# Optimization experiments

Measured on AMD Instinct MI355X. Metric: run time of the kernel, lower is better.

Reference implementation:

```python
import jax, jax.numpy as jnp
import numpy as np

N = 100000   # nodes (src == dst count)
E = 800000   # edges
D = 64       # hidden_dim == out_channels per head
H = 4        # heads
ED = 2       # edge_dim
NEG_SLOPE = 0.2
EPS = 1e-16


def setup_inputs() -> dict:
    key = jax.random.key(0)
    ks = jax.random.split(key, 12)
    s = 1.0 / np.sqrt(D)
    return {
        "x_src": jax.random.normal(ks[0], (N, D), jnp.float32),
        "x_dst": jax.random.normal(ks[1], (N, D), jnp.float32),
        "edge_index": jax.random.randint(ks[2], (2, E), 0, N),
        "edge_attr": jax.random.normal(ks[3], (E, ED), jnp.float32),
        "gamma": jnp.ones((D,), jnp.float32),
        "beta": jnp.zeros((D,), jnp.float32),
        "W_l": jax.random.normal(ks[4], (D, H * D), jnp.float32) * s,
        "b_l": jnp.zeros((H * D,), jnp.float32),
        "W_r": jax.random.normal(ks[5], (D, H * D), jnp.float32) * s,
        "b_r": jnp.zeros((H * D,), jnp.float32),
        "W_e": jax.random.normal(ks[6], (ED, H * D), jnp.float32) * s,
        "att": jax.random.normal(ks[7], (H, D), jnp.float32) * s,
        "bias": jnp.zeros((D,), jnp.float32),
    }


def _layernorm(x, gamma, beta):
    mu = jnp.mean(x, axis=-1, keepdims=True)
    var = jnp.var(x, axis=-1, keepdims=True)
    return (x - mu) * jax.lax.rsqrt(var + 1e-5) * gamma + beta


def reference(x_src, x_dst, edge_index, edge_attr, gamma, beta,
              W_l, b_l, W_r, b_r, W_e, att, bias):
    # shared LayerNorm on both bipartite node sets
    xs = _layernorm(x_src, gamma, beta)
    xd = _layernorm(x_dst, gamma, beta)
    # per-node linear transforms -> [N, H, D]
    hl = (xs @ W_l + b_l).reshape(N, H, D)   # source transform
    hr = (xd @ W_r + b_r).reshape(N, H, D)   # destination transform
    he = (edge_attr @ W_e).reshape(E, H, D)  # edge transform (no bias)
    src, dst = edge_index[0], edge_index[1]
    # GATv2 score: LeakyReLU(x_j + x_i + e) . att
    m = jax.nn.leaky_relu(hl[src] + hr[dst] + he, NEG_SLOPE)  # [E, H, D]
    alpha = jnp.einsum('ehd,hd->eh', m, att)                  # [E, H]
    # segment softmax over edges sharing a destination
    amax = jax.ops.segment_max(alpha, dst, num_segments=N)    # [N, H]
    ex = jnp.exp(alpha - amax[dst])
    denom = jax.ops.segment_sum(ex, dst, num_segments=N)      # [N, H]
    alpha = ex / (denom[dst] + EPS)
    # scatter-aggregate messages x_j * alpha
    out = jax.ops.segment_sum(hl[src] * alpha[..., None], dst, num_segments=N)  # [N, H, D]
    # concat=False -> mean over heads, then bias
    return out.mean(axis=1) + bias
```

## Files before the change

kernel.cpp:

```cpp
#include <hip/hip_runtime.h>
#include <hip/hip_bf16.h>
#include <cstdint>

#define NN 100000
#define EE 800000
#define DD 64
#define HH 4
#define HDIM 256
#define NEG 0.2f
#define L2E 1.4426950408889634f
#define CAP 44
#define HLMASK 0x03FFFFF8

#define NGB ((NN + 63) / 64)
#define GEMM_BLOCKS (NGB * 2)
#define SCAT_BLOCKS ((EE + 255) / 256)
#define SCAT4_BLOCKS ((EE + 1023) / 1024)
#define TOTAL_BLOCKS (SCAT4_BLOCKS * 5)

typedef __attribute__((ext_vector_type(8))) short bf16x8;
typedef __attribute__((ext_vector_type(4))) float f32x4;
typedef __attribute__((ext_vector_type(2))) float f32x2;

__device__ __forceinline__ float bf2f(unsigned short u) {
  union { unsigned int i; float f; } c; c.i = ((unsigned int)u) << 16; return c.f;
}
__device__ __forceinline__ unsigned short f2bf(float f) {
  union { float f; unsigned int i; } c; c.f = f;
  unsigned int r = c.i + 0x7FFF + ((c.i >> 16) & 1);
  return (unsigned short)(r >> 16);
}
__device__ __forceinline__ unsigned int pack2(unsigned short a, unsigned short b) {
  return (unsigned int)a | ((unsigned int)b << 16);
}
__device__ __forceinline__ f32x2 unpk(unsigned int u) {
  union { unsigned int i; float f; } lo, hi;
  lo.i = u << 16; hi.i = u & 0xffff0000u;
  f32x2 r; r.x = lo.f; r.y = hi.f; return r;
}
__device__ __forceinline__ f32x2 abs2(f32x2 a) {
  f32x2 r; r.x = fmaxf(a.x, -a.x); r.y = fmaxf(a.y, -a.y); return r;
}

#if __has_builtin(__builtin_amdgcn_exp2f)
#define EXP2F(x) __builtin_amdgcn_exp2f(x)
#else
#define EXP2F(x) exp2f(x)
#endif

#define ROWSUM16(p) do {                                                         \
  p += __int_as_float(__builtin_amdgcn_update_dpp(0, __float_as_int(p), 0x121, 0xF, 0xF, false)); \
  p += __int_as_float(__builtin_amdgcn_update_dpp(0, __float_as_int(p), 0x122, 0xF, 0xF, false)); \
  p += __int_as_float(__builtin_amdgcn_update_dpp(0, __float_as_int(p), 0x124, 0xF, 0xF, false)); \
  p += __int_as_float(__builtin_amdgcn_update_dpp(0, __float_as_int(p), 0x128, 0xF, 0xF, false)); \
} while (0)

#define CIDX(l) ((((l) >> 4) << 6) + (((l) & 3) << 4) + ((((l) >> 2) & 3) << 2))

__device__ __forceinline__ void prep_body(
    int mat,
    const float* __restrict__ W_l, const float* __restrict__ b_l,
    const float* __restrict__ W_r, const float* __restrict__ b_r,
    const float* __restrict__ gamma, const float* __restrict__ beta,
    unsigned short* __restrict__ Wgt, float* __restrict__ cw,
    float* __restrict__ cb)
{
  const int c = threadIdx.x;
  const float* W = mat ? W_r : W_l;
  const float* bb = mat ? b_r : b_l;
  unsigned short* wout = Wgt + (size_t)mat * HDIM * DD + (size_t)c * DD;
  float s_cw = 0.f, s_cb = 0.f;
#pragma unroll 8
  for (int k = 0; k < DD; ++k) {
    float wv = W[k * HDIM + c];
    unsigned short u = f2bf(gamma[k] * wv);
    wout[k] = u;
    s_cw += bf2f(u);
    s_cb += beta[k] * wv;
  }
  cw[mat * HDIM + c] = s_cw;
  cb[mat * HDIM + c] = s_cb + bb[c];
}

__global__ __launch_bounds__(256) void k_prep(
    const float* __restrict__ W_l, const float* __restrict__ b_l,
    const float* __restrict__ W_r, const float* __restrict__ b_r,
    const float* __restrict__ gamma, const float* __restrict__ beta,
    unsigned short* __restrict__ Wgt, float* __restrict__ cw,
    float* __restrict__ cb, int* __restrict__ deg)
{
  if (blockIdx.x < 2) {
    prep_body(blockIdx.x, W_l, b_l, W_r, b_r, gamma, beta, Wgt, cw, cb);
    return;
  }
  int i = (blockIdx.x - 2) * 256 + threadIdx.x;
  if (i < NN) deg[i] = 0;
}

__device__ __forceinline__ void gemm_body(
    int gx,
    const float* __restrict__ x_src, const float* __restrict__ x_dst,
    const unsigned short* __restrict__ Wgt, const float* __restrict__ cw,
    const float* __restrict__ cb,
    unsigned short* __restrict__ hl, unsigned short* __restrict__ hr)
{
  const int mat = gx & 1;
  const int tile = gx >> 1;
  const int t = threadIdx.x;
  const float* __restrict__ xp = mat ? x_dst : x_src;
  unsigned short* __restrict__ HM = mat ? hr : hl;

  __shared__ __align__(16) unsigned short sh[2][64 * 72];
  __shared__ float smu[64], sinv[64];

  const int l = t & 63, w = t >> 6;
  const int row16 = l & 15, hq = l >> 4;
  const int c0 = w * 64;

  const int sr = t >> 2, sq = t & 3;
  float v[16];
  {
    const int n = tile * 64 + sr;
    if (n < NN) {
      const f32x4* xr = (const f32x4*)(xp + (size_t)n * DD + sq * 16);
#pragma unroll
      for (int j = 0; j < 4; ++j) {
        f32x4 f = __builtin_nontemporal_load(xr + j);
        v[4 * j + 0] = f.x; v[4 * j + 1] = f.y;
        v[4 * j + 2] = f.z; v[4 * j + 3] = f.w;
      }
    } else {
#pragma unroll
      for (int j = 0; j < 16; ++j) v[j] = 0.f;
    }
  }

  const unsigned short* WgtM = Wgt + (size_t)mat * HDIM * DD;
  bf16x8 bfr[4][2];
#pragma unroll
  for (int cbk = 0; cbk < 4; ++cbk)
#pragma unroll
    for (int kb = 0; kb < 2; ++kb)
      bfr[cbk][kb] = *(const bf16x8*)(WgtM + (size_t)(c0 + cbk * 16 + row16) * DD
                                      + kb * 32 + hq * 8);
  float4 cw4[4], cb4[4];
#pragma unroll
  for (int cbk = 0; cbk < 4; ++cbk) {
    cw4[cbk] = *(const float4*)(cw + mat * HDIM + c0 + cbk * 16 + hq * 4);
    cb4[cbk] = *(const float4*)(cb + mat * HDIM + c0 + cbk * 16 + hq * 4);
  }

  {
    float s = 0.f, s2 = 0.f;
#pragma unroll
    for (int j = 0; j < 16; ++j) { s += v[j]; s2 += v[j] * v[j]; }
    s  += __shfl_xor(s, 1, 64);  s  += __shfl_xor(s, 2, 64);
    s2 += __shfl_xor(s2, 1, 64); s2 += __shfl_xor(s2, 2, 64);
    const float mu = s * (1.0f / DD);
    const float var = s2 * (1.0f / DD) - mu * mu;
    const float inv = rsqrtf(var + 1e-5f);
    if (sq == 0) { smu[sr] = mu; sinv[sr] = inv; }
    unsigned short hi[16], lo[16];
#pragma unroll
    for (int j = 0; j < 16; ++j) {
      unsigned short h = f2bf(v[j]);
      hi[j] = h;
      lo[j] = f2bf(v[j] - bf2f(h));
    }
    const int base = sr * 72 + sq * 16;
    uint4 w0, w1;
    w0.x = pack2(hi[0], hi[1]);  w0.y = pack2(hi[2], hi[3]);
    w0.z = pack2(hi[4], hi[5]);  w0.w = pack2(hi[6], hi[7]);
    w1.x = pack2(hi[8], hi[9]);  w1.y = pack2(hi[10], hi[11]);
    w1.z = pack2(hi[12], hi[13]); w1.w = pack2(hi[14], hi[15]);
    *(uint4*)(&sh[0][base]) = w0;
    *(uint4*)(&sh[0][base + 8]) = w1;
    w0.x = pack2(lo[0], lo[1]);  w0.y = pack2(lo[2], lo[3]);
    w0.z = pack2(lo[4], lo[5]);  w0.w = pack2(lo[6], lo[7]);
    w1.x = pack2(lo[8], lo[9]);  w1.y = pack2(lo[10], lo[11]);
    w1.z = pack2(lo[12], lo[13]); w1.w = pack2(lo[14], lo[15]);
    *(uint4*)(&sh[1][base]) = w0;
    *(uint4*)(&sh[1][base + 8]) = w1;
  }
  __syncthreads();

#pragma unroll
  for (int rb = 0; rb < 4; ++rb) {
    const int abase = (rb * 16 + row16) * 72 + hq * 8;
    bf16x8 xh0 = *(const bf16x8*)(&sh[0][abase]);
    bf16x8 xh1 = *(const bf16x8*)(&sh[0][abase + 32]);
    bf16x8 xl0 = *(const bf16x8*)(&sh[1][abase]);
    bf16x8 xl1 = *(const bf16x8*)(&sh[1][abase + 32]);
    f32x4 acc[4];
#pragma unroll
    for (int cbk = 0; cbk < 4; ++cbk) {
      acc[cbk] = (f32x4){0.f, 0.f, 0.f, 0.f};
      acc[cbk] = __builtin_amdgcn_mfma_f32_16x16x32_bf16(bfr[cbk][0], xh0, acc[cbk], 0, 0, 0);
      acc[cbk] = __builtin_amdgcn_mfma_f32_16x16x32_bf16(bfr[cbk][1], xh1, acc[cbk], 0, 0, 0);
      acc[cbk] = __builtin_amdgcn_mfma_f32_16x16x32_bf16(bfr[cbk][0], xl0, acc[cbk], 0, 0, 0);
      acc[cbk] = __builtin_amdgcn_mfma_f32_16x16x32_bf16(bfr[cbk][1], xl1, acc[cbk], 0, 0, 0);
    }
    const int nloc = rb * 16 + row16;
    const int node = tile * 64 + nloc;
    const float mu = smu[nloc], inv = sinv[nloc];
    if (node < NN) {
      float hh[4][4];
#pragma unroll
      for (int cbk = 0; cbk < 4; ++cbk) {
        hh[cbk][0] = fmaf(-mu, cw4[cbk].x, acc[cbk][0]) * inv + cb4[cbk].x;
        hh[cbk][1] = fmaf(-mu, cw4[cbk].y, acc[cbk][1]) * inv + cb4[cbk].y;
        hh[cbk][2] = fmaf(-mu, cw4[cbk].z, acc[cbk][2]) * inv + cb4[cbk].z;
        hh[cbk][3] = fmaf(-mu, cw4[cbk].w, acc[cbk][3]) * inv + cb4[cbk].w;
      }
      unsigned short* rp = HM + (size_t)node * HDIM + c0 + hq * 16;
      uint4 s0, s1;
      s0.x = pack2(f2bf(hh[0][0]), f2bf(hh[0][1]));
      s0.y = pack2(f2bf(hh[0][2]), f2bf(hh[0][3]));
      s0.z = pack2(f2bf(hh[1][0]), f2bf(hh[1][1]));
      s0.w = pack2(f2bf(hh[1][2]), f2bf(hh[1][3]));
      s1.x = pack2(f2bf(hh[2][0]), f2bf(hh[2][1]));
      s1.y = pack2(f2bf(hh[2][2]), f2bf(hh[2][3]));
      s1.z = pack2(f2bf(hh[3][0]), f2bf(hh[3][1]));
      s1.w = pack2(f2bf(hh[3][2]), f2bf(hh[3][3]));
      *(uint4*)rp = s0;
      *(uint4*)(rp + 8) = s1;
    }
  }
}

__device__ __forceinline__ void scatter_body4(
    int bx, const int* __restrict__ ei, const float* __restrict__ eattr,
    int* __restrict__ deg, int2* __restrict__ epack)
{
  const int e0 = bx * 1024 + threadIdx.x;
  int src[4], dst[4];
  unsigned long long ea[4];
  bool ok[4];
#pragma unroll
  for (int k = 0; k < 4; ++k) {
    const int e = e0 + k * 256;
    ok[k] = (e < EE);
    const int es = ok[k] ? e : 0;
    src[k] = __builtin_nontemporal_load(ei + es);
    dst[k] = __builtin_nontemporal_load(ei + EE + es);
    ea[k]  = __builtin_nontemporal_load((const unsigned long long*)(eattr + 2 * es));
  }
  int slot[4];
#pragma unroll
  for (int k = 0; k < 4; ++k) {
    if (ok[k]) slot[k] = atomicAdd(&deg[dst[k]], 1);
    else slot[k] = CAP;
  }
#pragma unroll
  for (int k = 0; k < 4; ++k) {
    if (slot[k] < CAP) {
      const float eax = __uint_as_float((unsigned int)ea[k]);
      const float eay = __uint_as_float((unsigned int)(ea[k] >> 32));
      unsigned long long rec =
          (unsigned long long)(unsigned int)(src[k] << 9)
          | ((unsigned long long)pack2(f2bf(eax), f2bf(eay)) << 32);
      __builtin_nontemporal_store(
          rec, (unsigned long long*)(epack + (size_t)dst[k] * CAP + slot[k]));
    }
  }
}

__global__ __launch_bounds__(256) void k_gemm_scatter(
    const float* __restrict__ x_src, const float* __restrict__ x_dst,
    const unsigned short* __restrict__ Wgt, const float* __restrict__ cw,
    const float* __restrict__ cb,
    unsigned short* __restrict__ hl, unsigned short* __restrict__ hr,
    const int* __restrict__ ei, const float* __restrict__ eattr,
    int* __restrict__ deg, int2* __restrict__ epack)
{
  const int bx = blockIdx.x;
  const int q = bx / 5, r = bx - q * 5;
  if (r == 4) {
    scatter_body4(q, ei, eattr, deg, epack);
  } else {
    const int g = q * 4 + r;
    if (g < GEMM_BLOCKS)
      gemm_body(g, x_src, x_dst, Wgt, cw, cb, hl, hr);
  }
}

__global__ __launch_bounds__(256, 8) void k_agg(
    const int* __restrict__ deg,
    const unsigned short* __restrict__ hl, const unsigned short* __restrict__ hr,
    const float* __restrict__ W_e, const float* __restrict__ att,
    const float* __restrict__ bias, const int2* __restrict__ epack,
    float* __restrict__ out)
{
  const int t = threadIdx.x;
  const int l = t & 63;
  const int loff = l * 8;
  const int cidx = CIDX(l);
  const char* hlb = (const char*)hl;

  const float4 at4 = *(const float4*)(att + cidx);
  const float4 w0  = *(const float4*)(W_e + cidx);
  const float4 w1  = *(const float4*)(W_e + HDIM + cidx);
  f32x2 atA01, atA23, atB01, atB23, w001, w023, w101, w123;
  atA01.x = at4.x * (0.6f * L2E); atA01.y = at4.y * (0.6f * L2E);
  atA23.x = at4.z * (0.6f * L2E); atA23.y = at4.w * (0.6f * L2E);
  atB01.x = at4.x * (0.4f * L2E); atB01.y = at4.y * (0.4f * L2E);
  atB23.x = at4.z * (0.4f * L2E); atB23.y = at4.w * (0.4f * L2E);
  w001.x = w0.x; w001.y = w0.y; w023.x = w0.z; w023.y = w0.w;
  w101.x = w1.x; w101.y = w1.y; w123.x = w1.z; w123.y = w1.w;

  const int nwaves = gridDim.x * (blockDim.x >> 6);
  const int wid0 = blockIdx.x * (blockDim.x >> 6) + (t >> 6);
  for (int n = wid0; n < NN; n += nwaves) {
    const int nu = __builtin_amdgcn_readfirstlane(n);
    int cnt = __builtin_amdgcn_readfirstlane(deg[nu]);
    cnt = min(cnt, CAP);
    const uint2 hv = *(const uint2*)(hr + (size_t)nu * HDIM + l * 4);
    const f32x2 r01 = unpk(hv.x), r23 = unpk(hv.y);
    f32x2 acc01 = {0.f, 0.f}, acc23 = {0.f, 0.f};
    float den = 0.f;

    auto EDGE = [&](int ey, uint2 av) {
      const f32x2 eav = unpk((unsigned int)ey);
      const f32x2 a01 = unpk(av.x), a23 = unpk(av.y);
      f32x2 s01 = a01 + r01 + w001 * eav.x + w101 * eav.y;
      f32x2 s23 = a23 + r23 + w023 * eav.x + w123 * eav.y;
      f32x2 q = s01 * atA01 + abs2(s01) * atB01;
      q = q + s23 * atA23 + abs2(s23) * atB23;
      float p = q.x + q.y;
      ROWSUM16(p);
      const float ex = EXP2F(p);
      acc01 += a01 * ex;
      acc23 += a23 * ex;
      den += ex;
    };

    if (cnt > 0) {
      const int2* eptr = epack + (size_t)nu * CAP;
      int2 e0 = eptr[0], e1 = eptr[1], e2 = eptr[2], e3 = eptr[3],
           e4 = eptr[4], e5 = eptr[5], e6 = eptr[6], e7 = eptr[7];
      uint2 a0 = *(const uint2*)(hlb + (e0.x & HLMASK) + loff);
      uint2 a1 = *(const uint2*)(hlb + (e1.x & HLMASK) + loff);
      uint2 a2 = *(const uint2*)(hlb + (e2.x & HLMASK) + loff);
      uint2 a3 = *(const uint2*)(hlb + (e3.x & HLMASK) + loff);
      int i = 0;
      for (; i + 4 <= cnt; i += 4) {
        uint2 b4 = *(const uint2*)(hlb + (e4.x & HLMASK) + loff);
        uint2 b5 = *(const uint2*)(hlb + (e5.x & HLMASK) + loff);
        uint2 b6 = *(const uint2*)(hlb + (e6.x & HLMASK) + loff);
        uint2 b7 = *(const uint2*)(hlb + (e7.x & HLMASK) + loff);
        int2 t0 = eptr[i + 8], t1 = eptr[i + 9],
             t2 = eptr[i + 10], t3 = eptr[i + 11];
        EDGE(e0.y, a0);
        EDGE(e1.y, a1);
        EDGE(e2.y, a2);
        EDGE(e3.y, a3);
        e0 = e4; e1 = e5; e2 = e6; e3 = e7;
        e4 = t0; e5 = t1; e6 = t2; e7 = t3;
        a0 = b4; a1 = b5; a2 = b6; a3 = b7;
      }
      const int rem = cnt - i;
      if (rem > 0) EDGE(e0.y, a0);
      if (rem > 1) EDGE(e1.y, a1);
      if (rem > 2) EDGE(e2.y, a2);
    }

    const float inv = 1.0f / (den + 1e-16f);
    float v0 = acc01.x * inv, v1 = acc01.y * inv;
    float v2 = acc23.x * inv, v3 = acc23.y * inv;
    v0 += __shfl_xor(v0, 16, 64); v0 += __shfl_xor(v0, 32, 64);
    v1 += __shfl_xor(v1, 16, 64); v1 += __shfl_xor(v1, 32, 64);
    v2 += __shfl_xor(v2, 16, 64); v2 += __shfl_xor(v2, 32, 64);
    v3 += __shfl_xor(v3, 16, 64); v3 += __shfl_xor(v3, 32, 64);
    if (l < 16) {
      const float4 bias4 = *(const float4*)(bias + cidx);
      float4 o;
      o.x = 0.25f * v0 + bias4.x;
      o.y = 0.25f * v1 + bias4.y;
      o.z = 0.25f * v2 + bias4.z;
      o.w = 0.25f * v3 + bias4.w;
      *(float4*)(out + (size_t)nu * DD + cidx) = o;
    }
  }
}

__global__ __launch_bounds__(256) void k_prep_count(
    const float* __restrict__ W_l, const float* __restrict__ b_l,
    const float* __restrict__ W_r, const float* __restrict__ b_r,
    const float* __restrict__ gamma, const float* __restrict__ beta,
    unsigned short* __restrict__ Wgt, float* __restrict__ cw,
    float* __restrict__ cb,
    const int* __restrict__ ei, int* __restrict__ counts)
{
  if (blockIdx.x < 2) {
    prep_body(blockIdx.x, W_l, b_l, W_r, b_r, gamma, beta, Wgt, cw, cb);
  } else {
    int e = (blockIdx.x - 2) * 256 + threadIdx.x;
    if (e < EE) atomicAdd(&counts[ei[EE + e]], 1);
  }
}

__global__ __launch_bounds__(256) void k_base(const int* __restrict__ counts,
                                              int* __restrict__ cursor,
                                              int* __restrict__ rowstart,
                                              int* __restrict__ cur) {
  const int lane = threadIdx.x & 63;
  const int wid = (blockIdx.x * blockDim.x + threadIdx.x) >> 6;
  const int n = wid * 64 + lane;
  int val = (n < NN) ? counts[n] : 0;
  int s = val;
#pragma unroll
  for (int off = 1; off < 64; off <<= 1) {
    int tsh = __shfl_up(s, off, 64);
    if (lane >= off) s += tsh;
  }
  int total = __shfl(s, 63, 64);
  int base = 0;
  if (lane == 0) base = atomicAdd(cursor, total);
  base = __shfl(base, 0, 64);
  if (n < NN) {
    int rs = base + s - val;
    rowstart[n] = rs;
    cur[n] = rs;
  }
}

__global__ __launch_bounds__(256) void k_scatter_csr(const int* __restrict__ ei,
                                                     const float* __restrict__ eattr,
                                                     int* __restrict__ cur,
                                                     int2* __restrict__ epack) {
  int e = blockIdx.x * blockDim.x + threadIdx.x;
  if (e >= EE) return;
  if (e < 64) epack[EE + e] = make_int2(0, 0);
  int src = ei[e];
  int dst = ei[EE + e];
  float2 ea = *(const float2*)(eattr + 2 * e);
  int pos = atomicAdd(&cur[dst], 1);
  epack[pos] = make_int2(src << 9, (int)pack2(f2bf(ea.x), f2bf(ea.y)));
}

__global__ __launch_bounds__(256, 8) void k_agg_csr(
    const int* __restrict__ rowstart, const int* __restrict__ counts,
    const unsigned short* __restrict__ hl, const unsigned short* __restrict__ hr,
    const float* __restrict__ W_e, const float* __restrict__ att,
    const float* __restrict__ bias, const int2* __restrict__ epack,
    float* __restrict__ out)
{
  const int t = threadIdx.x;
  const int l = t & 63;
  const int loff = l * 8;
  const int cidx = CIDX(l);
  const char* hlb = (const char*)hl;
  const float4 at4 = *(const float4*)(att + cidx);
  const float4 w0  = *(const float4*)(W_e + cidx);
  const float4 w1  = *(const float4*)(W_e + HDIM + cidx);
  f32x2 atA01, atA23, atB01, atB23, w001, w023, w101, w123;
  atA01.x = at4.x * (0.6f * L2E); atA01.y = at4.y * (0.6f * L2E);
  atA23.x = at4.z * (0.6f * L2E); atA23.y = at4.w * (0.6f * L2E);
  atB01.x = at4.x * (0.4f * L2E); atB01.y = at4.y * (0.4f * L2E);
  atB23.x = at4.z * (0.4f * L2E); atB23.y = at4.w * (0.4f * L2E);
  w001.x = w0.x; w001.y = w0.y; w023.x = w0.z; w023.y = w0.w;
  w101.x = w1.x; w101.y = w1.y; w123.x = w1.z; w123.y = w1.w;
  const int nwaves = gridDim.x * (blockDim.x >> 6);
  const int wid0 = blockIdx.x * (blockDim.x >> 6) + (t >> 6);
  for (int n = wid0; n < NN; n += nwaves) {
    const int nu = __builtin_amdgcn_readfirstlane(n);
    const int start = __builtin_amdgcn_readfirstlane(rowstart[nu]);
    const int cnt = __builtin_amdgcn_readfirstlane(counts[nu]);
    const uint2 hv = *(const uint2*)(hr + (size_t)nu * HDIM + l * 4);
    const f32x2 r01 = unpk(hv.x), r23 = unpk(hv.y);
    f32x2 acc01 = {0.f, 0.f}, acc23 = {0.f, 0.f};
    float den = 0.f;
    for (int i = 0; i < cnt; ++i) {
      int2 ep = epack[start + i];
      uint2 av = *(const uint2*)(hlb + (ep.x & HLMASK) + loff);
      const f32x2 eav = unpk((unsigned int)ep.y);
      const f32x2 a01 = unpk(av.x), a23 = unpk(av.y);
      f32x2 s01 = a01 + r01 + w001 * eav.x + w101 * eav.y;
      f32x2 s23 = a23 + r23 + w023 * eav.x + w123 * eav.y;
      f32x2 q = s01 * atA01 + abs2(s01) * atB01;
      q = q + s23 * atA23 + abs2(s23) * atB23;
      float p = q.x + q.y;
      ROWSUM16(p);
      const float ex = EXP2F(p);
      acc01 += a01 * ex;
      acc23 += a23 * ex;
      den += ex;
    }
    const float inv = 1.0f / (den + 1e-16f);
    float v0 = acc01.x * inv, v1 = acc01.y * inv;
    float v2 = acc23.x * inv, v3 = acc23.y * inv;
    v0 += __shfl_xor(v0, 16, 64); v0 += __shfl_xor(v0, 32, 64);
    v1 += __shfl_xor(v1, 16, 64); v1 += __shfl_xor(v1, 32, 64);
    v2 += __shfl_xor(v2, 16, 64); v2 += __shfl_xor(v2, 32, 64);
    v3 += __shfl_xor(v3, 16, 64); v3 += __shfl_xor(v3, 32, 64);
    if (l < 16) {
      const float4 bias4 = *(const float4*)(bias + cidx);
      float4 o;
      o.x = 0.25f * v0 + bias4.x;
      o.y = 0.25f * v1 + bias4.y;
      o.z = 0.25f * v2 + bias4.z;
      o.w = 0.25f * v3 + bias4.w;
      *(float4*)(out + (size_t)nu * DD + cidx) = o;
    }
  }
}

__global__ __launch_bounds__(256) void k_gemm_only(
    const float* __restrict__ x_src, const float* __restrict__ x_dst,
    const unsigned short* __restrict__ Wgt, const float* __restrict__ cw,
    const float* __restrict__ cb,
    unsigned short* __restrict__ hl, unsigned short* __restrict__ hr)
{
  gemm_body(blockIdx.x, x_src, x_dst, Wgt, cw, cb, hl, hr);
}

extern "C" void kernel_launch(void* const* d_in, const int* in_sizes, int n_in,
                              void* d_out, int out_size, void* d_ws, size_t ws_size,
                              hipStream_t stream) {
  const float* x_src = (const float*)d_in[0];
  const float* x_dst = (const float*)d_in[1];
  const int*   ei    = (const int*)d_in[2];
  const float* eattr = (const float*)d_in[3];
  const float* gamma = (const float*)d_in[4];
  const float* beta  = (const float*)d_in[5];
  const float* W_l   = (const float*)d_in[6];
  const float* b_l   = (const float*)d_in[7];
  const float* W_r   = (const float*)d_in[8];
  const float* b_r   = (const float*)d_in[9];
  const float* W_e   = (const float*)d_in[10];
  const float* att   = (const float*)d_in[11];
  const float* bias  = (const float*)d_in[12];
  float* out = (float*)d_out;

  char* ws = (char*)d_ws;
  unsigned short* hl = (unsigned short*)ws;
  unsigned short* hr = hl + (size_t)NN * HDIM;
  char* rest = (char*)(hr + (size_t)NN * HDIM);

  const size_t fixed_need = (size_t)NN * HDIM * 2 * 2
                          + ((size_t)NN * CAP + 64) * 8
                          + 2 * HDIM * DD * 2 + 4 * HDIM * 4
                          + (size_t)NN * 4 + 4096;

  if (ws_size >= fixed_need) {
    int2* epack = (int2*)rest;
    unsigned short* Wgt = (unsigned short*)(epack + (size_t)NN * CAP + 64);
    float* cw = (float*)(Wgt + 2 * HDIM * DD);
    float* cb = cw + 2 * HDIM;
    int* deg = (int*)(cb + 2 * HDIM);

    k_prep<<<2 + (NN + 255) / 256, 256, 0, stream>>>(
        W_l, b_l, W_r, b_r, gamma, beta, Wgt, cw, cb, deg);
    k_gemm_scatter<<<TOTAL_BLOCKS, 256, 0, stream>>>(
        x_src, x_dst, Wgt, cw, cb, hl, hr, ei, eattr, deg, epack);
    k_agg<<<2048, 256, 0, stream>>>(deg, hl, hr, W_e, att, bias, epack, out);
  } else {
    int2* epack = (int2*)rest;
    unsigned short* Wgt = (unsigned short*)(epack + EE + 64);
    float* cw = (float*)(Wgt + 2 * HDIM * DD);
    float* cb = cw + 2 * HDIM;
    int* counts   = (int*)(cb + 2 * HDIM);
    int* cursor   = counts + NN;
    int* rowstart = cursor + 1;
    int* cur      = rowstart + NN;

    hipMemsetAsync(counts, 0, (size_t)(NN + 1) * sizeof(int), stream);
    k_prep_count<<<2 + SCAT_BLOCKS, 256, 0, stream>>>(
        W_l, b_l, W_r, b_r, gamma, beta, Wgt, cw, cb, ei, counts);
    k_base<<<(NGB * 64 + 255) / 256, 256, 0, stream>>>(
        counts, cursor, rowstart, cur);
    k_gemm_only<<<GEMM_BLOCKS, 256, 0, stream>>>(
        x_src, x_dst, Wgt, cw, cb, hl, hr);
    k_scatter_csr<<<SCAT_BLOCKS, 256, 0, stream>>>(ei, eattr, cur, epack);
    k_agg_csr<<<2048, 256, 0, stream>>>(rowstart, counts, hl, hr, W_e, att,
                                        bias, epack, out);
  }
}
```

Measured before the change: 152.7 us.

## Software-pipeline node loop: prefetch next node's edges, hr row and degrees

```diff
diff --git a/kernel.cpp b/kernel.cpp
--- a/kernel.cpp
+++ b/kernel.cpp
@@ -310,12 +310,41 @@
 
   const int nwaves = gridDim.x * (blockDim.x >> 6);
   const int wid0 = blockIdx.x * (blockDim.x >> 6) + (t >> 6);
-  for (int n = wid0; n < NN; n += nwaves) {
-    const int nu = __builtin_amdgcn_readfirstlane(n);
-    int cnt = __builtin_amdgcn_readfirstlane(deg[nu]);
-    cnt = min(cnt, CAP);
-    const uint2 hv = *(const uint2*)(hr + (size_t)nu * HDIM + l * 4);
-    const f32x2 r01 = unpk(hv.x), r23 = unpk(hv.y);
+  if (wid0 >= NN) return;
+
+  int pdeg = 0;
+  {
+    const int pn = wid0 + l * nwaves;
+    if (pn < NN) pdeg = deg[pn];
+  }
+
+  int n = wid0;
+  int cnt = min(__shfl(pdeg, 0), CAP);
+  const int2* eptr = epack + (size_t)n * CAP;
+  int2 e0 = eptr[0], e1 = eptr[1], e2 = eptr[2], e3 = eptr[3],
+       e4 = eptr[4], e5 = eptr[5], e6 = eptr[6], e7 = eptr[7];
+  unsigned long long hvv =
+      __builtin_nontemporal_load((const unsigned long long*)(hr + (size_t)n * HDIM + l * 4));
+
+  int it = 0;
+  for (;;) {
+    uint2 a0 = *(const uint2*)(hlb + ((0 < cnt) ? (e0.x & HLMASK) : 0) + loff);
+    uint2 a1 = *(const uint2*)(hlb + ((1 < cnt) ? (e1.x & HLMASK) : 0) + loff);
+    uint2 a2 = *(const uint2*)(hlb + ((2 < cnt) ? (e2.x & HLMASK) : 0) + loff);
+    uint2 a3 = *(const uint2*)(hlb + ((3 < cnt) ? (e3.x & HLMASK) : 0) + loff);
+
+    const int n2 = n + nwaves;
+    ++it;
+    const int ns = (n2 < NN) ? n2 : 0;
+    int cnt2 = min(__shfl(pdeg, min(it, 63)), CAP);
+    if (n2 >= NN) cnt2 = 0;
+    const int2* eptr2 = epack + (size_t)ns * CAP;
+    int2 f0 = eptr2[0], f1 = eptr2[1], f2 = eptr2[2], f3 = eptr2[3],
+         f4 = eptr2[4], f5 = eptr2[5], f6 = eptr2[6], f7 = eptr2[7];
+    unsigned long long hvv2 =
+        __builtin_nontemporal_load((const unsigned long long*)(hr + (size_t)ns * HDIM + l * 4));
+
+    const f32x2 r01 = unpk((unsigned int)hvv), r23 = unpk((unsigned int)(hvv >> 32));
     f32x2 acc01 = {0.f, 0.f}, acc23 = {0.f, 0.f};
     float den = 0.f;
 
@@ -335,19 +364,12 @@
     };
 
     if (cnt > 0) {
-      const int2* eptr = epack + (size_t)nu * CAP;
-      int2 e0 = eptr[0], e1 = eptr[1], e2 = eptr[2], e3 = eptr[3],
-           e4 = eptr[4], e5 = eptr[5], e6 = eptr[6], e7 = eptr[7];
-      uint2 a0 = *(const uint2*)(hlb + (e0.x & HLMASK) + loff);
-      uint2 a1 = *(const uint2*)(hlb + (e1.x & HLMASK) + loff);
-      uint2 a2 = *(const uint2*)(hlb + (e2.x & HLMASK) + loff);
-      uint2 a3 = *(const uint2*)(hlb + (e3.x & HLMASK) + loff);
       int i = 0;
       for (; i + 4 <= cnt; i += 4) {
-        uint2 b4 = *(const uint2*)(hlb + (e4.x & HLMASK) + loff);
-        uint2 b5 = *(const uint2*)(hlb + (e5.x & HLMASK) + loff);
-        uint2 b6 = *(const uint2*)(hlb + (e6.x & HLMASK) + loff);
-        uint2 b7 = *(const uint2*)(hlb + (e7.x & HLMASK) + loff);
+        uint2 b4 = *(const uint2*)(hlb + ((i + 4 < cnt) ? (e4.x & HLMASK) : 0) + loff);
+        uint2 b5 = *(const uint2*)(hlb + ((i + 5 < cnt) ? (e5.x & HLMASK) : 0) + loff);
+        uint2 b6 = *(const uint2*)(hlb + ((i + 6 < cnt) ? (e6.x & HLMASK) : 0) + loff);
+        uint2 b7 = *(const uint2*)(hlb + ((i + 7 < cnt) ? (e7.x & HLMASK) : 0) + loff);
         int2 t0 = eptr[i + 8], t1 = eptr[i + 9],
              t2 = eptr[i + 10], t3 = eptr[i + 11];
         EDGE(e0.y, a0);
@@ -373,13 +395,19 @@
     v3 += __shfl_xor(v3, 16, 64); v3 += __shfl_xor(v3, 32, 64);
     if (l < 16) {
       const float4 bias4 = *(const float4*)(bias + cidx);
-      float4 o;
+      f32x4 o;
       o.x = 0.25f * v0 + bias4.x;
       o.y = 0.25f * v1 + bias4.y;
       o.z = 0.25f * v2 + bias4.z;
       o.w = 0.25f * v3 + bias4.w;
-      *(float4*)(out + (size_t)nu * DD + cidx) = o;
-    }
+      __builtin_nontemporal_store(o, (f32x4*)(out + (size_t)n * DD + cidx));
+    }
+
+    if (n2 >= NN) break;
+    n = n2; cnt = cnt2; eptr = eptr2;
+    e0 = f0; e1 = f1; e2 = f2; e3 = f3;
+    e4 = f4; e5 = f5; e6 = f6; e7 = f7;
+    hvv = hvv2;
   }
 }
 
```

New measurement: 546.6 us. 258% more time.
